# Performance work log

Measured on AMD Instinct MI355X. Metric: run time of the kernel, lower is better.

The kernel has to match this reference:

```python
import jax, jax.numpy as jnp
import numpy as np

B, N, D, E, ET, L = 2, 50000, 64, 400000, 200000, 6
R_STRUCT = 4
EPS = 1e-5


def _ln(x, g, b):
    m = jnp.mean(x, axis=-1, keepdims=True)
    v = jnp.mean((x - m) ** 2, axis=-1, keepdims=True)
    return (x - m) * jax.lax.rsqrt(v + EPS) * g + b


def _nbf(boundary, src, dst, rel_e_fn, W, b, g, beta):
    # One RelNBFNet / TextRelNBFNet stack of GeneralizedRelationalConv layers:
    #   distmult message, sum aggregation with boundary self-loop message,
    #   linear([x, agg]) -> layernorm -> relu, short_cut residual.
    # boundary: [B, N, D]
    x = boundary
    for i in range(W.shape[0]):
        msg = x[:, src, :] * rel_e_fn(i)                    # [B, E, D]
        agg = jnp.zeros_like(x).at[:, dst, :].add(msg) + boundary
        h = jnp.concatenate([x, agg], axis=-1) @ W[i] + b[i]
        h = jax.nn.relu(_ln(h, g[i], beta[i]))
        x = h + x                                           # short_cut
    return x


def setup_inputs() -> dict:
    key = jax.random.key(0)
    ks = jax.random.split(key, 16)
    s = 0.05
    return {
        "rel_text_init": jax.random.normal(ks[0], (N, D), jnp.float32),
        "struct_rel": jax.random.normal(ks[1], (L, R_STRUCT, D), jnp.float32) * s,
        "struct_W": jax.random.normal(ks[2], (L, 2 * D, D), jnp.float32) * s,
        "struct_b": jnp.zeros((L, D), jnp.float32),
        "struct_g": jnp.ones((L, D), jnp.float32),
        "struct_beta": jnp.zeros((L, D), jnp.float32),
        "text_rel": jax.random.normal(ks[3], (L, 1, D), jnp.float32) * s,
        "text_W": jax.random.normal(ks[4], (L, 2 * D, D), jnp.float32) * s,
        "text_b": jnp.zeros((L, D), jnp.float32),
        "text_g": jnp.ones((L, D), jnp.float32),
        "text_beta": jnp.zeros((L, D), jnp.float32),
        "fuse_W1": jax.random.normal(ks[5], (2 * D, D), jnp.float32) * s,
        "fuse_b1": jnp.zeros((D,), jnp.float32),
        "fuse_W2": jax.random.normal(ks[6], (D, D), jnp.float32) * s,
        "fuse_b2": jnp.zeros((D,), jnp.float32),
        "h_index": jax.random.randint(ks[7], (B,), 0, N),
        "edge_index": jax.random.randint(ks[8], (2, E), 0, N),
        "edge_type": jax.random.randint(ks[9], (E,), 0, R_STRUCT),
        "text_edge_index": jax.random.randint(ks[10], (2, ET), 0, N),
    }


def reference(rel_text_init, struct_rel, struct_W, struct_b, struct_g, struct_beta,
              text_rel, text_W, text_b, text_g, text_beta,
              fuse_W1, fuse_b1, fuse_W2, fuse_b2,
              h_index, edge_index, edge_type, text_edge_index):
    # struct branch: boundary = indicator at query relation node
    boundary_s = jnp.zeros((B, N, D), rel_text_init.dtype).at[jnp.arange(B), h_index].add(1.0)
    h = _nbf(boundary_s, edge_index[0], edge_index[1],
             lambda i: struct_rel[i][edge_type],
             struct_W, struct_b, struct_g, struct_beta)
    # text branch: boundary = text-derived init features, single relation type
    boundary_t = jnp.broadcast_to(rel_text_init[None], (B, N, D))
    z = _nbf(boundary_t, text_edge_index[0], text_edge_index[1],
             lambda i: text_rel[i, 0][None, None, :],
             text_W, text_b, text_g, text_beta)
    # mlp fusion (alpha = 1.0)
    f = jax.nn.relu(jnp.concatenate([h, z], axis=-1) @ fuse_W1 + fuse_b1)
    return f @ fuse_W2 + fuse_b2
```

## Files before the change

### kernel.cpp

```cpp
#include <hip/hip_runtime.h>


__device__ __forceinline__ float bf2f(unsigned short u) {
    return __uint_as_float(((unsigned)u) << 16);
}
__device__ __forceinline__ unsigned short f2bf(float f) {
    unsigned u = __float_as_uint(f);
    u += 0x7FFF + ((u >> 16) & 1);
    return (unsigned short)(u >> 16);
}
#define PACK2(a, b) ((unsigned)f2bf(a) | ((unsigned)f2bf(b) << 16))

#define FMA4R(v, wbase, R0, R1, R2, R3) do {                                  \
    const float4* _w = (const float4*)(wbase); float4 _t;                     \
    _t=_w[0]; R0.x=fmaf(v,_t.x,R0.x); R0.y=fmaf(v,_t.y,R0.y); R0.z=fmaf(v,_t.z,R0.z); R0.w=fmaf(v,_t.w,R0.w); \
    _t=_w[1]; R1.x=fmaf(v,_t.x,R1.x); R1.y=fmaf(v,_t.y,R1.y); R1.z=fmaf(v,_t.z,R1.z); R1.w=fmaf(v,_t.w,R1.w); \
    _t=_w[2]; R2.x=fmaf(v,_t.x,R2.x); R2.y=fmaf(v,_t.y,R2.y); R2.z=fmaf(v,_t.z,R2.z); R2.w=fmaf(v,_t.w,R2.w); \
    _t=_w[3]; R3.x=fmaf(v,_t.x,R3.x); R3.y=fmaf(v,_t.y,R3.y); R3.z=fmaf(v,_t.z,R3.z); R3.w=fmaf(v,_t.w,R3.w); \
} while (0)

#define FMA4R2(v0, v1, wbase, P0,P1,P2,P3, Q0,Q1,Q2,Q3) do {                  \
    const float4* _w = (const float4*)(wbase); float4 _t;                     \
    _t=_w[0];                                                                 \
    P0.x=fmaf(v0,_t.x,P0.x); P0.y=fmaf(v0,_t.y,P0.y); P0.z=fmaf(v0,_t.z,P0.z); P0.w=fmaf(v0,_t.w,P0.w); \
    Q0.x=fmaf(v1,_t.x,Q0.x); Q0.y=fmaf(v1,_t.y,Q0.y); Q0.z=fmaf(v1,_t.z,Q0.z); Q0.w=fmaf(v1,_t.w,Q0.w); \
    _t=_w[1];                                                                 \
    P1.x=fmaf(v0,_t.x,P1.x); P1.y=fmaf(v0,_t.y,P1.y); P1.z=fmaf(v0,_t.z,P1.z); P1.w=fmaf(v0,_t.w,P1.w); \
    Q1.x=fmaf(v1,_t.x,Q1.x); Q1.y=fmaf(v1,_t.y,Q1.y); Q1.z=fmaf(v1,_t.z,Q1.z); Q1.w=fmaf(v1,_t.w,Q1.w); \
    _t=_w[2];                                                                 \
    P2.x=fmaf(v0,_t.x,P2.x); P2.y=fmaf(v0,_t.y,P2.y); P2.z=fmaf(v0,_t.z,P2.z); P2.w=fmaf(v0,_t.w,P2.w); \
    Q2.x=fmaf(v1,_t.x,Q2.x); Q2.y=fmaf(v1,_t.y,Q2.y); Q2.z=fmaf(v1,_t.z,Q2.z); Q2.w=fmaf(v1,_t.w,Q2.w); \
    _t=_w[3];                                                                 \
    P3.x=fmaf(v0,_t.x,P3.x); P3.y=fmaf(v0,_t.y,P3.y); P3.z=fmaf(v0,_t.z,P3.z); P3.w=fmaf(v0,_t.w,P3.w); \
    Q3.x=fmaf(v1,_t.x,Q3.x); Q3.y=fmaf(v1,_t.y,Q3.y); Q3.z=fmaf(v1,_t.z,Q3.z); Q3.w=fmaf(v1,_t.w,Q3.w); \
} while (0)

#define SUM4(Ai) ((Ai.x + Ai.y) + (Ai.z + Ai.w))
#define VAR4M(Ai, mm, vv) do { float _c;                                      \
    _c = Ai.x - mm; vv = fmaf(_c, _c, vv); _c = Ai.y - mm; vv = fmaf(_c, _c, vv); \
    _c = Ai.z - mm; vv = fmaf(_c, _c, vv); _c = Ai.w - mm; vv = fmaf(_c, _c, vv); \
} while (0)

#define RSEL(ty) (((ty) < 2) ? ((ty) == 0 ? r0 : r1) : ((ty) == 2 ? r2 : r3))

__global__ __launch_bounds__(256) void k_init_onehot(
    float* __restrict__ x, unsigned short* __restrict__ xbf,
    const int* __restrict__ h_index, int N, int total)
{
    int idx = blockIdx.x * 256 + threadIdx.x;
    if (idx >= total) return;
    int row = idx >> 6;
    int b = row / N;
    int n = row - b * N;
    bool hit = (n == h_index[b]);
    x[idx] = hit ? 1.0f : 0.0f;
    xbf[idx] = hit ? 0x3F80 : 0;
}

__global__ __launch_bounds__(256) void k_cast_init(
    const float* __restrict__ init, float* __restrict__ x,
    unsigned short* __restrict__ xbf, int total)
{
    int idx = blockIdx.x * 256 + threadIdx.x;
    if (idx >= total) return;
    float f = init[idx];
    x[idx] = f;
    xbf[idx] = f2bf(f);
}

__global__ __launch_bounds__(256) void k_hist_all(
    const int* __restrict__ dst_s, const int* __restrict__ dst_t,
    int* __restrict__ cnt_s, int* __restrict__ cnt_t, int E, int ET)
{
    int i = blockIdx.x * 256 + threadIdx.x;
    if (i < E) atomicAdd(&cnt_s[dst_s[i]], 1);
    else if (i < E + ET) atomicAdd(&cnt_t[dst_t[i - E]], 1);
}

__global__ __launch_bounds__(1024) void k_scan_blk2(
    const int* __restrict__ cnt_s, int* __restrict__ off_s, int* __restrict__ bsum_s,
    const int* __restrict__ cnt_t, int* __restrict__ off_t, int* __restrict__ bsum_t,
    int n, int nb)
{
    bool tpath = blockIdx.x >= nb;
    int lb = tpath ? blockIdx.x - nb : blockIdx.x;
    const int* cnt = tpath ? cnt_t : cnt_s;
    int* off = tpath ? off_t : off_s;
    int* bsum = tpath ? bsum_t : bsum_s;

    __shared__ int wsum[16], wpre[16], tot;
    int tid = threadIdx.x, lane = tid & 63, w = tid >> 6;
    int i = lb * 1024 + tid;
    int v = (i < n) ? cnt[i] : 0;
    int s = v;
    #pragma unroll
    for (int d = 1; d < 64; d <<= 1) {
        int t = __shfl_up(s, d);
        if (lane >= d) s += t;
    }
    if (lane == 63) wsum[w] = s;
    __syncthreads();
    if (w == 0 && lane < 16) {
        int ws = wsum[lane];
        int p = ws;
        #pragma unroll
        for (int d = 1; d < 16; d <<= 1) {
            int t = __shfl_up(p, d);
            if (lane >= d) p += t;
        }
        wpre[lane] = p - ws;
        if (lane == 15) tot = p;
    }
    __syncthreads();
    if (i < n) off[i + 1] = wpre[w] + s;
    if (tid == 0) {
        bsum[lb] = tot;
        if (lb == 0) off[0] = 0;
    }
}

__global__ __launch_bounds__(1024) void k_scan_top2(
    int* __restrict__ bsum_s, int* __restrict__ bsum_t, int nb)
{
    int* bsum = (blockIdx.x == 0) ? bsum_s : bsum_t;
    __shared__ int wsum[16], wpre[16];
    int tid = threadIdx.x, lane = tid & 63, w = tid >> 6;
    int v = (tid < nb) ? bsum[tid] : 0;
    int s = v;
    #pragma unroll
    for (int d = 1; d < 64; d <<= 1) {
        int t = __shfl_up(s, d);
        if (lane >= d) s += t;
    }
    if (lane == 63) wsum[w] = s;
    __syncthreads();
    if (w == 0 && lane < 16) {
        int ws = wsum[lane];
        int p = ws;
        #pragma unroll
        for (int d = 1; d < 16; d <<= 1) {
            int t = __shfl_up(p, d);
            if (lane >= d) p += t;
        }
        wpre[lane] = p - ws;
    }
    __syncthreads();
    if (tid < nb) bsum[tid] = wpre[w] + s - v;
}

__global__ __launch_bounds__(1024) void k_scan_add2(
    const int* __restrict__ bsum_s, int* __restrict__ off_s,
    const int* __restrict__ bsum_t, int* __restrict__ off_t, int n, int nb)
{
    bool tpath = blockIdx.x >= nb;
    int lb = tpath ? blockIdx.x - nb : blockIdx.x;
    int i = lb * 1024 + threadIdx.x;
    if (i < n) (tpath ? off_t : off_s)[i + 1] += (tpath ? bsum_t : bsum_s)[lb];
}

__global__ __launch_bounds__(256) void k_fill_all(
    const int* __restrict__ src_s, const int* __restrict__ dst_s,
    const int* __restrict__ etype,
    const int* __restrict__ off_s, int* __restrict__ cnt_s, int* __restrict__ pk_s,
    const int* __restrict__ src_t, const int* __restrict__ dst_t,
    const int* __restrict__ off_t, int* __restrict__ cnt_t, int* __restrict__ pk_t,
    int E, int ET)
{
    int i = blockIdx.x * 256 + threadIdx.x;
    if (i < E) {
        int d = dst_s[i];
        int pos = off_s[d] + atomicSub(&cnt_s[d], 1) - 1;
        pk_s[pos] = src_s[i] | (etype[i] << 27);
    } else if (i < E + ET) {
        int e = i - E;
        int d = dst_t[e];
        int pos = off_t[d] + atomicSub(&cnt_t[d], 1) - 1;
        pk_t[pos] = src_t[e];
    }
}

__global__ __launch_bounds__(256) void k_gather_all(
    const unsigned short* __restrict__ xbs, float* __restrict__ aggs,
    const int* __restrict__ offs, const int* __restrict__ pks,
    const float* __restrict__ rels,
    const int* __restrict__ hidx,
    const unsigned short* __restrict__ xbt, float* __restrict__ aggt,
    const int* __restrict__ offt, const int* __restrict__ pkt,
    const float* __restrict__ relt,
    const float* __restrict__ init,
    int N, int sblocks, int tblocks)
{
    int tid = threadIdx.x;
    int lane = tid & 63;
    bool isStruct; int lb;
    if (sblocks == tblocks) { isStruct = !(blockIdx.x & 1); lb = blockIdx.x >> 1; }
    else if ((int)blockIdx.x < sblocks) { isStruct = true; lb = blockIdx.x; }
    else { isStruct = false; lb = blockIdx.x - sblocks; }
    int n = (lb * 256 + tid) >> 6;
    if (n >= N) return;

    if (isStruct) {
        float r0 = rels[lane], r1 = rels[64 + lane];
        float r2 = rels[128 + lane], r3 = rels[192 + lane];
        const unsigned short* x0 = xbs;
        const unsigned short* x1 = xbs + (size_t)N * 64;
        float acc0 = (n == hidx[0]) ? 1.0f : 0.0f;
        float acc1 = (n == hidx[1]) ? 1.0f : 0.0f;
        int p0 = __builtin_amdgcn_readfirstlane(offs[n]);
        int p1 = __builtin_amdgcn_readfirstlane(offs[n + 1]);
        for (int p = p0; p < p1; p += 64) {
            int myPk = (p + lane < p1) ? pks[p + lane] : 0;
            int cnt = min(p1 - p, 64);
            int i = 0;
            for (; i + 4 <= cnt; i += 4) {
                int pka = __shfl(myPk, i + 0), pkb = __shfl(myPk, i + 1);
                int pkc = __shfl(myPk, i + 2), pkd = __shfl(myPk, i + 3);
                int sa = pka & 0x03FFFFFF, ta = pka >> 27;
                int sb = pkb & 0x03FFFFFF, tb = pkb >> 27;
                int sc = pkc & 0x03FFFFFF, tc = pkc >> 27;
                int sd = pkd & 0x03FFFFFF, td = pkd >> 27;
                float ra = RSEL(ta), rb = RSEL(tb), rc = RSEL(tc), rd = RSEL(td);
                float a0 = bf2f(x0[(size_t)sa * 64 + lane]), a1 = bf2f(x1[(size_t)sa * 64 + lane]);
                float b0 = bf2f(x0[(size_t)sb * 64 + lane]), b1 = bf2f(x1[(size_t)sb * 64 + lane]);
                float c0 = bf2f(x0[(size_t)sc * 64 + lane]), c1 = bf2f(x1[(size_t)sc * 64 + lane]);
                float d0 = bf2f(x0[(size_t)sd * 64 + lane]), d1 = bf2f(x1[(size_t)sd * 64 + lane]);
                acc0 = fmaf(a0, ra, acc0); acc1 = fmaf(a1, ra, acc1);
                acc0 = fmaf(b0, rb, acc0); acc1 = fmaf(b1, rb, acc1);
                acc0 = fmaf(c0, rc, acc0); acc1 = fmaf(c1, rc, acc1);
                acc0 = fmaf(d0, rd, acc0); acc1 = fmaf(d1, rd, acc1);
            }
            for (; i < cnt; ++i) {
                int pk = __shfl(myPk, i);
                int s = pk & 0x03FFFFFF, ty = pk >> 27;
                float r = RSEL(ty);
                acc0 = fmaf(bf2f(x0[(size_t)s * 64 + lane]), r, acc0);
                acc1 = fmaf(bf2f(x1[(size_t)s * 64 + lane]), r, acc1);
            }
        }
        aggs[(size_t)n * 64 + lane] = acc0;
        aggs[(size_t)(N + n) * 64 + lane] = acc1;
    } else {
        float r = relt[lane];
        float acc = init[(size_t)n * 64 + lane];
        float acc2 = 0.f;
        int p0 = __builtin_amdgcn_readfirstlane(offt[n]);
        int p1 = __builtin_amdgcn_readfirstlane(offt[n + 1]);
        for (int p = p0; p < p1; p += 64) {
            int myPk = (p + lane < p1) ? pkt[p + lane] : 0;
            int cnt = min(p1 - p, 64);
            int i = 0;
            for (; i + 8 <= cnt; i += 8) {
                int s0 = __shfl(myPk, i + 0), s1 = __shfl(myPk, i + 1);
                int s2 = __shfl(myPk, i + 2), s3 = __shfl(myPk, i + 3);
                int s4 = __shfl(myPk, i + 4), s5 = __shfl(myPk, i + 5);
                int s6 = __shfl(myPk, i + 6), s7 = __shfl(myPk, i + 7);
                float a = bf2f(xbt[(size_t)s0 * 64 + lane]), b = bf2f(xbt[(size_t)s1 * 64 + lane]);
                float c = bf2f(xbt[(size_t)s2 * 64 + lane]), d = bf2f(xbt[(size_t)s3 * 64 + lane]);
                float e = bf2f(xbt[(size_t)s4 * 64 + lane]), f = bf2f(xbt[(size_t)s5 * 64 + lane]);
                float g = bf2f(xbt[(size_t)s6 * 64 + lane]), h = bf2f(xbt[(size_t)s7 * 64 + lane]);
                acc = fmaf(a, r, acc);  acc2 = fmaf(b, r, acc2);
                acc = fmaf(c, r, acc);  acc2 = fmaf(d, r, acc2);
                acc = fmaf(e, r, acc);  acc2 = fmaf(f, r, acc2);
                acc = fmaf(g, r, acc);  acc2 = fmaf(h, r, acc2);
            }
            for (; i < cnt; ++i) {
                int s = __shfl(myPk, i);
                acc = fmaf(bf2f(xbt[(size_t)s * 64 + lane]), r, acc);
            }
        }
        aggt[(size_t)n * 64 + lane] = acc + acc2;
    }
}

__global__ __launch_bounds__(256) void k_gather_struct_gen(
    const float* __restrict__ x, float* __restrict__ agg,
    const int* __restrict__ off, const int* __restrict__ packed,
    const float* __restrict__ rel, const int* __restrict__ h_index,
    int N, int BN)
{
    int wid = (blockIdx.x * 256 + threadIdx.x) >> 6;
    int lane = threadIdx.x & 63;
    if (wid >= BN) return;
    int b = wid / N;
    int n = wid - b * N;
    float r0 = rel[lane], r1 = rel[64 + lane];
    float r2 = rel[128 + lane], r3 = rel[192 + lane];
    const float* xb = x + (size_t)b * N * 64;
    float acc = (n == h_index[b]) ? 1.0f : 0.0f;
    int p0 = off[n], p1 = off[n + 1];
    for (int p = p0; p < p1; ++p) {
        int pk = packed[p];
        int s = pk & 0x03FFFFFF, ty = pk >> 27;
        acc = fmaf(xb[(size_t)s * 64 + lane], RSEL(ty), acc);
    }
    agg[(size_t)wid * 64 + lane] = acc;
}

__global__ __launch_bounds__(256) void k_update_all(
    const float* __restrict__ Ws, const float* __restrict__ bs_,
    const float* __restrict__ gs, const float* __restrict__ betas,
    float* __restrict__ xs, unsigned short* __restrict__ xbs,
    const float* __restrict__ aggs, int rows_s,
    const float* __restrict__ Wt, const float* __restrict__ bt_,
    const float* __restrict__ gt_, const float* __restrict__ betat,
    float* __restrict__ xt, unsigned short* __restrict__ xbt,
    const float* __restrict__ aggt, int rows_t,
    int bs_blocks, int bt_blocks)
{
    bool tpath; int lb;
    if (bs_blocks == 2 * bt_blocks) {
        int m3 = blockIdx.x % 3, d3 = blockIdx.x / 3;
        if (m3 != 2) { tpath = false; lb = d3 * 2 + m3; }
        else { tpath = true; lb = d3; }
    } else if ((int)blockIdx.x < bs_blocks) { tpath = false; lb = blockIdx.x; }
    else { tpath = true; lb = blockIdx.x - bs_blocks; }

    const float* W    = tpath ? Wt : Ws;
    const float* bias = tpath ? bt_ : bs_;
    const float* g    = tpath ? gt_ : gs;
    const float* beta = tpath ? betat : betas;
    float* x          = tpath ? xt : xs;
    unsigned short* xb = tpath ? xbt : xbs;
    const float* agg  = tpath ? aggt : aggs;
    int rows          = tpath ? rows_t : rows_s;

    __shared__ float Wl[128 * 64];
    __shared__ float bl[64], gl[64], bel[64];
    int tid = threadIdx.x;
    {
        const float4* W4 = (const float4*)W;
        float4* Wl4 = (float4*)Wl;
        #pragma unroll
        for (int i = 0; i < 8; ++i) Wl4[tid + i * 256] = W4[tid + i * 256];
        if (tid < 64) { bl[tid] = bias[tid]; gl[tid] = g[tid]; bel[tid] = beta[tid]; }
    }
    __syncthreads();

    int gt2 = lb * 256 + tid;
    int pair = gt2 >> 2;
    int q = gt2 & 3, jc = q * 16;
    int r0i = pair * 2, r1i = r0i + 1;
    if (r0i >= rows) return;
    bool h1 = (r1i < rows);
    const float* xr0 = x + (size_t)r0i * 64;
    const float* ar0 = agg + (size_t)r0i * 64;
    const float* xr1 = h1 ? x + (size_t)r1i * 64 : xr0;
    const float* ar1 = h1 ? agg + (size_t)r1i * 64 : ar0;

    const float4* bj = (const float4*)(bl + jc);
    float4 A0 = bj[0], A1 = bj[1], A2 = bj[2], A3 = bj[3];
    float4 B0 = bj[0], B1 = bj[1], B2 = bj[2], B3 = bj[3];

    #pragma unroll
    for (int kb = 0; kb < 64; kb += 4) {
        float4 i0 = *(const float4*)(xr0 + kb);
        float4 i1 = *(const float4*)(xr1 + kb);
        FMA4R2(i0.x, i1.x, Wl + (kb + 0) * 64 + jc, A0,A1,A2,A3, B0,B1,B2,B3);
        FMA4R2(i0.y, i1.y, Wl + (kb + 1) * 64 + jc, A0,A1,A2,A3, B0,B1,B2,B3);
        FMA4R2(i0.z, i1.z, Wl + (kb + 2) * 64 + jc, A0,A1,A2,A3, B0,B1,B2,B3);
        FMA4R2(i0.w, i1.w, Wl + (kb + 3) * 64 + jc, A0,A1,A2,A3, B0,B1,B2,B3);
    }
    #pragma unroll
    for (int kb = 0; kb < 64; kb += 4) {
        float4 i0 = *(const float4*)(ar0 + kb);
        float4 i1 = *(const float4*)(ar1 + kb);
        FMA4R2(i0.x, i1.x, Wl + (64 + kb + 0) * 64 + jc, A0,A1,A2,A3, B0,B1,B2,B3);
        FMA4R2(i0.y, i1.y, Wl + (64 + kb + 1) * 64 + jc, A0,A1,A2,A3, B0,B1,B2,B3);
        FMA4R2(i0.z, i1.z, Wl + (64 + kb + 2) * 64 + jc, A0,A1,A2,A3, B0,B1,B2,B3);
        FMA4R2(i0.w, i1.w, Wl + (64 + kb + 3) * 64 + jc, A0,A1,A2,A3, B0,B1,B2,B3);
    }

    float ls0 = SUM4(A0) + SUM4(A1) + SUM4(A2) + SUM4(A3);
    float ls1 = SUM4(B0) + SUM4(B1) + SUM4(B2) + SUM4(B3);
    ls0 += __shfl_xor(ls0, 1); ls0 += __shfl_xor(ls0, 2);
    ls1 += __shfl_xor(ls1, 1); ls1 += __shfl_xor(ls1, 2);
    float m0 = ls0 * (1.0f / 64.0f), m1 = ls1 * (1.0f / 64.0f);
    float v0 = 0.f, v1 = 0.f;
    VAR4M(A0, m0, v0); VAR4M(A1, m0, v0); VAR4M(A2, m0, v0); VAR4M(A3, m0, v0);
    VAR4M(B0, m1, v1); VAR4M(B1, m1, v1); VAR4M(B2, m1, v1); VAR4M(B3, m1, v1);
    v0 += __shfl_xor(v0, 1); v0 += __shfl_xor(v0, 2);
    v1 += __shfl_xor(v1, 1); v1 += __shfl_xor(v1, 2);
    float inv0 = rsqrtf(v0 * (1.0f / 64.0f) + 1e-5f);
    float inv1 = rsqrtf(v1 * (1.0f / 64.0f) + 1e-5f);

    const float4* gg4 = (const float4*)(gl + jc);
    const float4* bb4 = (const float4*)(bel + jc);
    #define OUTC(Aj, c, mm, iv, xrp, xwp, xbm) do {                           \
        float4 xv = ((const float4*)(xrp))[c];                                \
        float4 gg = gg4[c]; float4 bb = bb4[c];                               \
        float4 y;                                                             \
        y.x = fmaxf((Aj.x - mm) * iv * gg.x + bb.x, 0.f) + xv.x;              \
        y.y = fmaxf((Aj.y - mm) * iv * gg.y + bb.y, 0.f) + xv.y;              \
        y.z = fmaxf((Aj.z - mm) * iv * gg.z + bb.z, 0.f) + xv.z;              \
        y.w = fmaxf((Aj.w - mm) * iv * gg.w + bb.w, 0.f) + xv.w;              \
        ((float4*)(xwp))[c] = y;                                              \
        ((uint2*)(xbm))[c] = make_uint2(PACK2(y.x, y.y), PACK2(y.z, y.w));    \
    } while (0)
    float* xw0 = x + (size_t)r0i * 64 + jc;
    unsigned short* xb0 = xb + (size_t)r0i * 64 + jc;
    OUTC(A0, 0, m0, inv0, xr0 + jc, xw0, xb0); OUTC(A1, 1, m0, inv0, xr0 + jc, xw0, xb0);
    OUTC(A2, 2, m0, inv0, xr0 + jc, xw0, xb0); OUTC(A3, 3, m0, inv0, xr0 + jc, xw0, xb0);
    if (h1) {
        float* xw1 = x + (size_t)r1i * 64 + jc;
        unsigned short* xb1 = xb + (size_t)r1i * 64 + jc;
        OUTC(B0, 0, m1, inv1, xr1 + jc, xw1, xb1); OUTC(B1, 1, m1, inv1, xr1 + jc, xw1, xb1);
        OUTC(B2, 2, m1, inv1, xr1 + jc, xw1, xb1); OUTC(B3, 3, m1, inv1, xr1 + jc, xw1, xb1);
    }
    #undef OUTC
}

__global__ __launch_bounds__(256) void k_fuse(
    const float* __restrict__ W1, const float* __restrict__ b1,
    const float* __restrict__ W2, const float* __restrict__ b2,
    float* __restrict__ out, const float* __restrict__ z, int N, int rows)
{
    __shared__ float W1l[128 * 64];
    __shared__ float W2l[64 * 64];
    __shared__ float b1l[64], b2l[64];
    int tid = threadIdx.x;
    {
        const float4* Wa = (const float4*)W1;
        float4* Wla = (float4*)W1l;
        #pragma unroll
        for (int i = 0; i < 8; ++i) Wla[tid + i * 256] = Wa[tid + i * 256];
        const float4* Wb = (const float4*)W2;
        float4* Wlb = (float4*)W2l;
        #pragma unroll
        for (int i = 0; i < 4; ++i) Wlb[tid + i * 256] = Wb[tid + i * 256];
        if (tid < 64) { b1l[tid] = b1[tid]; b2l[tid] = b2[tid]; }
    }
    __syncthreads();

    int gt2 = blockIdx.x * 256 + tid;
    int row = gt2 >> 2;
    int q = gt2 & 3;
    int jc = q * 16;
    if (row >= rows) return;
    int n = row % N;
    const float* hr = out + (size_t)row * 64;
    const float* zr = z + (size_t)n * 64;
    int lane = tid & 63;

    const float4* bj = (const float4*)(b1l + jc);
    float4 F0 = bj[0], F1 = bj[1], F2 = bj[2], F3 = bj[3];
    #pragma unroll
    for (int kb = 0; kb < 64; kb += 4) {
        float4 iv = *(const float4*)(hr + kb);
        FMA4R(iv.x, W1l + (kb + 0) * 64 + jc, F0, F1, F2, F3);
        FMA4R(iv.y, W1l + (kb + 1) * 64 + jc, F0, F1, F2, F3);
        FMA4R(iv.z, W1l + (kb + 2) * 64 + jc, F0, F1, F2, F3);
        FMA4R(iv.w, W1l + (kb + 3) * 64 + jc, F0, F1, F2, F3);
    }
    #pragma unroll
    for (int kb = 0; kb < 64; kb += 4) {
        float4 iv = *(const float4*)(zr + kb);
        FMA4R(iv.x, W1l + (64 + kb + 0) * 64 + jc, F0, F1, F2, F3);
        FMA4R(iv.y, W1l + (64 + kb + 1) * 64 + jc, F0, F1, F2, F3);
        FMA4R(iv.z, W1l + (64 + kb + 2) * 64 + jc, F0, F1, F2, F3);
        FMA4R(iv.w, W1l + (64 + kb + 3) * 64 + jc, F0, F1, F2, F3);
    }
    F0.x = fmaxf(F0.x, 0.f); F0.y = fmaxf(F0.y, 0.f); F0.z = fmaxf(F0.z, 0.f); F0.w = fmaxf(F0.w, 0.f);
    F1.x = fmaxf(F1.x, 0.f); F1.y = fmaxf(F1.y, 0.f); F1.z = fmaxf(F1.z, 0.f); F1.w = fmaxf(F1.w, 0.f);
    F2.x = fmaxf(F2.x, 0.f); F2.y = fmaxf(F2.y, 0.f); F2.z = fmaxf(F2.z, 0.f); F2.w = fmaxf(F2.w, 0.f);
    F3.x = fmaxf(F3.x, 0.f); F3.y = fmaxf(F3.y, 0.f); F3.z = fmaxf(F3.z, 0.f); F3.w = fmaxf(F3.w, 0.f);

    const float4* bj2 = (const float4*)(b2l + jc);
    float4 O0 = bj2[0], O1 = bj2[1], O2 = bj2[2], O3 = bj2[3];
    int srcLane = (lane & ~3) | ((q + 1) & 3);
    #pragma unroll
    for (int s = 0; s < 4; ++s) {
        int c = (q + s) & 3;
        const float* w2 = W2l + (c * 16) * 64 + jc;
        FMA4R(F0.x, w2 + 0 * 64,  O0, O1, O2, O3);
        FMA4R(F0.y, w2 + 1 * 64,  O0, O1, O2, O3);
        FMA4R(F0.z, w2 + 2 * 64,  O0, O1, O2, O3);
        FMA4R(F0.w, w2 + 3 * 64,  O0, O1, O2, O3);
        FMA4R(F1.x, w2 + 4 * 64,  O0, O1, O2, O3);
        FMA4R(F1.y, w2 + 5 * 64,  O0, O1, O2, O3);
        FMA4R(F1.z, w2 + 6 * 64,  O0, O1, O2, O3);
        FMA4R(F1.w, w2 + 7 * 64,  O0, O1, O2, O3);
        FMA4R(F2.x, w2 + 8 * 64,  O0, O1, O2, O3);
        FMA4R(F2.y, w2 + 9 * 64,  O0, O1, O2, O3);
        FMA4R(F2.z, w2 + 10 * 64, O0, O1, O2, O3);
        FMA4R(F2.w, w2 + 11 * 64, O0, O1, O2, O3);
        FMA4R(F3.x, w2 + 12 * 64, O0, O1, O2, O3);
        FMA4R(F3.y, w2 + 13 * 64, O0, O1, O2, O3);
        FMA4R(F3.z, w2 + 14 * 64, O0, O1, O2, O3);
        FMA4R(F3.w, w2 + 15 * 64, O0, O1, O2, O3);
        if (s < 3) {
            F0.x = __shfl(F0.x, srcLane); F0.y = __shfl(F0.y, srcLane);
            F0.z = __shfl(F0.z, srcLane); F0.w = __shfl(F0.w, srcLane);
            F1.x = __shfl(F1.x, srcLane); F1.y = __shfl(F1.y, srcLane);
            F1.z = __shfl(F1.z, srcLane); F1.w = __shfl(F1.w, srcLane);
            F2.x = __shfl(F2.x, srcLane); F2.y = __shfl(F2.y, srcLane);
            F2.z = __shfl(F2.z, srcLane); F2.w = __shfl(F2.w, srcLane);
            F3.x = __shfl(F3.x, srcLane); F3.y = __shfl(F3.y, srcLane);
            F3.z = __shfl(F3.z, srcLane); F3.w = __shfl(F3.w, srcLane);
        }
    }
    float4* ow4 = (float4*)(out + (size_t)row * 64 + jc);
    ow4[0] = O0; ow4[1] = O1; ow4[2] = O2; ow4[3] = O3;
}

extern "C" void kernel_launch(void* const* d_in, const int* in_sizes, int n_in,
                              void* d_out, int out_size, void* d_ws, size_t ws_size,
                              hipStream_t stream)
{
    const float* rel_text_init = (const float*)d_in[0];
    const float* struct_rel    = (const float*)d_in[1];
    const float* struct_W      = (const float*)d_in[2];
    const float* struct_b      = (const float*)d_in[3];
    const float* struct_g      = (const float*)d_in[4];
    const float* struct_beta   = (const float*)d_in[5];
    const float* text_rel      = (const float*)d_in[6];
    const float* text_W        = (const float*)d_in[7];
    const float* text_b        = (const float*)d_in[8];
    const float* text_g        = (const float*)d_in[9];
    const float* text_beta     = (const float*)d_in[10];
    const float* fuse_W1       = (const float*)d_in[11];
    const float* fuse_b1       = (const float*)d_in[12];
    const float* fuse_W2       = (const float*)d_in[13];
    const float* fuse_b2       = (const float*)d_in[14];
    const int*   h_index       = (const int*)d_in[15];
    const int*   edge_index    = (const int*)d_in[16];
    const int*   edge_type     = (const int*)d_in[17];
    const int*   text_edge_idx = (const int*)d_in[18];

    const int B  = in_sizes[15];
    const int N  = in_sizes[0] / 64;
    const int E  = in_sizes[17];
    const int ET = in_sizes[18] / 2;
    const int L  = in_sizes[3] / 64;
    const int R  = in_sizes[1] / (L * 64);

    const int* src  = edge_index;
    const int* dst  = edge_index + E;
    const int* tsrc = text_edge_idx;
    const int* tdst = text_edge_idx + ET;

    float* x_t   = (float*)d_ws;
    float* agg_t = x_t + (size_t)N * 64;
    float* agg_s = agg_t + (size_t)N * 64;
    unsigned short* xbf_s = (unsigned short*)(agg_s + (size_t)B * N * 64);
    unsigned short* xbf_t = xbf_s + (size_t)B * N * 64;
    int*   cnt_s = (int*)(xbf_t + (size_t)N * 64);
    int*   off_s = cnt_s + N;
    int*   pk_s  = off_s + N + 1;
    int*   cnt_t = pk_s + E;
    int*   off_t = cnt_t + N;
    int*   pk_t  = off_t + N + 1;
    int*   bsum_s = pk_t + ET;
    int*   bsum_t = bsum_s + 1024;

    float* x_s = (float*)d_out;

    const size_t nd  = (size_t)N * 64;
    const int rows_s = B * N;
    const int tot_s  = rows_s * 64;
    const int nb     = (N + 1023) / 1024;

    const int gb_init   = (tot_s + 255) / 256;
    const int gb_castt  = ((int)nd + 255) / 256;
    const int gb_hist   = (E + ET + 255) / 256;
    const int gb_wave_n = (N * 64 + 255) / 256;
    const int pairs_s   = (rows_s + 1) / 2;
    const int pairs_t   = (N + 1) / 2;
    const int bs_blocks = (pairs_s * 4 + 255) / 256;
    const int bt_blocks = (pairs_t * 4 + 255) / 256;
    const int gb_fuse   = (rows_s * 4 + 255) / 256;

    hipMemsetAsync(cnt_s, 0, (size_t)N * 4, stream);
    hipMemsetAsync(cnt_t, 0, (size_t)N * 4, stream);
    k_hist_all<<<gb_hist, 256, 0, stream>>>(dst, tdst, cnt_s, cnt_t, E, ET);
    k_scan_blk2<<<2 * nb, 1024, 0, stream>>>(cnt_s, off_s, bsum_s,
                                             cnt_t, off_t, bsum_t, N, nb);
    k_scan_top2<<<2, 1024, 0, stream>>>(bsum_s, bsum_t, nb);
    k_scan_add2<<<2 * nb, 1024, 0, stream>>>(bsum_s, off_s, bsum_t, off_t, N, nb);
    k_fill_all<<<gb_hist, 256, 0, stream>>>(src, dst, edge_type, off_s, cnt_s, pk_s,
                                            tsrc, tdst, off_t, cnt_t, pk_t, E, ET);

    k_init_onehot<<<gb_init, 256, 0, stream>>>(x_s, xbf_s, h_index, N, tot_s);
    k_cast_init<<<gb_castt, 256, 0, stream>>>(rel_text_init, x_t, xbf_t, (int)nd);

    for (int i = 0; i < L; ++i) {
        if (B == 2) {
            k_gather_all<<<2 * gb_wave_n, 256, 0, stream>>>(
                xbf_s, agg_s, off_s, pk_s, struct_rel + (size_t)i * R * 64, h_index,
                xbf_t, agg_t, off_t, pk_t, text_rel + (size_t)i * 64, rel_text_init,
                N, gb_wave_n, gb_wave_n);
        } else {
            k_gather_struct_gen<<<(rows_s * 64 + 255) / 256, 256, 0, stream>>>(
                x_s, agg_s, off_s, pk_s,
                struct_rel + (size_t)i * R * 64, h_index, N, rows_s);
            k_gather_all<<<gb_wave_n, 256, 0, stream>>>(
                xbf_s, agg_s, off_s, pk_s, struct_rel + (size_t)i * R * 64, h_index,
                xbf_t, agg_t, off_t, pk_t, text_rel + (size_t)i * 64, rel_text_init,
                N, 0, gb_wave_n);
        }
        k_update_all<<<bs_blocks + bt_blocks, 256, 0, stream>>>(
            struct_W + (size_t)i * 128 * 64, struct_b + i * 64,
            struct_g + i * 64, struct_beta + i * 64, x_s, xbf_s, agg_s, rows_s,
            text_W + (size_t)i * 128 * 64, text_b + i * 64,
            text_g + i * 64, text_beta + i * 64, x_t, xbf_t, agg_t, N,
            bs_blocks, bt_blocks);
    }

    k_fuse<<<gb_fuse, 256, 0, stream>>>(
        fuse_W1, fuse_b1, fuse_W2, fuse_b2, x_s, x_t, N, rows_s);
}
```

Baseline: 692.9 us.

## Interleave struct batch bf16 mirror so gather loads both batches in one word

The bf16 mirror of the struct-branch features changes from two separate batch planes to an interleaved layout where each node/channel holds both batches' values in one 32-bit word. The gather then issues one 4-byte load per edge instead of two 2-byte loads to distant planes, and its inner loop is unrolled to 8 edges for more memory-level parallelism. The update kernel now writes scattered 2-byte halves into the interleaved mirror, which may cost more write efficiency, and the init kernel builds the interleaved one-hot mirror.

Result: slower. 854.4 us (+23.3%).

```diff
diff --git a/kernel.cpp b/kernel.cpp
--- a/kernel.cpp
+++ b/kernel.cpp
@@ -10,6 +10,16 @@
     return (unsigned short)(u >> 16);
 }
 #define PACK2(a, b) ((unsigned)f2bf(a) | ((unsigned)f2bf(b) << 16))
+
+__device__ __forceinline__ float4 lnout(float4 A, float m, float inv,
+                                        float4 xv, float4 gg, float4 bb) {
+    float4 y;
+    y.x = fmaxf((A.x - m) * inv * gg.x + bb.x, 0.f) + xv.x;
+    y.y = fmaxf((A.y - m) * inv * gg.y + bb.y, 0.f) + xv.y;
+    y.z = fmaxf((A.z - m) * inv * gg.z + bb.z, 0.f) + xv.z;
+    y.w = fmaxf((A.w - m) * inv * gg.w + bb.w, 0.f) + xv.w;
+    return y;
+}
 
 #define FMA4R(v, wbase, R0, R1, R2, R3) do {                                  \
     const float4* _w = (const float4*)(wbase); float4 _t;                     \
@@ -44,17 +54,21 @@
 #define RSEL(ty) (((ty) < 2) ? ((ty) == 0 ? r0 : r1) : ((ty) == 2 ? r2 : r3))
 
 __global__ __launch_bounds__(256) void k_init_onehot(
-    float* __restrict__ x, unsigned short* __restrict__ xbf,
-    const int* __restrict__ h_index, int N, int total)
+    float* __restrict__ x, unsigned* __restrict__ xmir,
+    const int* __restrict__ h_index, int N, int total, int b2)
 {
     int idx = blockIdx.x * 256 + threadIdx.x;
     if (idx >= total) return;
     int row = idx >> 6;
     int b = row / N;
     int n = row - b * N;
-    bool hit = (n == h_index[b]);
-    x[idx] = hit ? 1.0f : 0.0f;
-    xbf[idx] = hit ? 0x3F80 : 0;
+    x[idx] = (n == h_index[b]) ? 1.0f : 0.0f;
+    if (b2 && idx < N * 64) {
+        int nn = idx >> 6;
+        unsigned w = ((nn == h_index[0]) ? 0x3F80u : 0u)
+                   | (((nn == h_index[1]) ? 0x3F80u : 0u) << 16);
+        xmir[idx] = w;
+    }
 }
 
 __global__ __launch_bounds__(256) void k_cast_init(
@@ -180,7 +194,7 @@
 }
 
 __global__ __launch_bounds__(256) void k_gather_all(
-    const unsigned short* __restrict__ xbs, float* __restrict__ aggs,
+    const unsigned* __restrict__ xws, float* __restrict__ aggs,
     const int* __restrict__ offs, const int* __restrict__ pks,
     const float* __restrict__ rels,
     const int* __restrict__ hidx,
@@ -202,8 +216,6 @@
     if (isStruct) {
         float r0 = rels[lane], r1 = rels[64 + lane];
         float r2 = rels[128 + lane], r3 = rels[192 + lane];
-        const unsigned short* x0 = xbs;
-        const unsigned short* x1 = xbs + (size_t)N * 64;
         float acc0 = (n == hidx[0]) ? 1.0f : 0.0f;
         float acc1 = (n == hidx[1]) ? 1.0f : 0.0f;
         int p0 = __builtin_amdgcn_readfirstlane(offs[n]);
@@ -212,29 +224,47 @@
             int myPk = (p + lane < p1) ? pks[p + lane] : 0;
             int cnt = min(p1 - p, 64);
             int i = 0;
-            for (; i + 4 <= cnt; i += 4) {
-                int pka = __shfl(myPk, i + 0), pkb = __shfl(myPk, i + 1);
-                int pkc = __shfl(myPk, i + 2), pkd = __shfl(myPk, i + 3);
-                int sa = pka & 0x03FFFFFF, ta = pka >> 27;
-                int sb = pkb & 0x03FFFFFF, tb = pkb >> 27;
-                int sc = pkc & 0x03FFFFFF, tc = pkc >> 27;
-                int sd = pkd & 0x03FFFFFF, td = pkd >> 27;
-                float ra = RSEL(ta), rb = RSEL(tb), rc = RSEL(tc), rd = RSEL(td);
-                float a0 = bf2f(x0[(size_t)sa * 64 + lane]), a1 = bf2f(x1[(size_t)sa * 64 + lane]);
-                float b0 = bf2f(x0[(size_t)sb * 64 + lane]), b1 = bf2f(x1[(size_t)sb * 64 + lane]);
-                float c0 = bf2f(x0[(size_t)sc * 64 + lane]), c1 = bf2f(x1[(size_t)sc * 64 + lane]);
-                float d0 = bf2f(x0[(size_t)sd * 64 + lane]), d1 = bf2f(x1[(size_t)sd * 64 + lane]);
-                acc0 = fmaf(a0, ra, acc0); acc1 = fmaf(a1, ra, acc1);
-                acc0 = fmaf(b0, rb, acc0); acc1 = fmaf(b1, rb, acc1);
-                acc0 = fmaf(c0, rc, acc0); acc1 = fmaf(c1, rc, acc1);
-                acc0 = fmaf(d0, rd, acc0); acc1 = fmaf(d1, rd, acc1);
+            for (; i + 8 <= cnt; i += 8) {
+                int k0 = __shfl(myPk, i + 0), k1 = __shfl(myPk, i + 1);
+                int k2 = __shfl(myPk, i + 2), k3 = __shfl(myPk, i + 3);
+                int k4 = __shfl(myPk, i + 4), k5 = __shfl(myPk, i + 5);
+                int k6 = __shfl(myPk, i + 6), k7 = __shfl(myPk, i + 7);
+                unsigned w0 = xws[(size_t)(k0 & 0x03FFFFFF) * 64 + lane];
+                unsigned w1 = xws[(size_t)(k1 & 0x03FFFFFF) * 64 + lane];
+                unsigned w2 = xws[(size_t)(k2 & 0x03FFFFFF) * 64 + lane];
+                unsigned w3 = xws[(size_t)(k3 & 0x03FFFFFF) * 64 + lane];
+                unsigned w4 = xws[(size_t)(k4 & 0x03FFFFFF) * 64 + lane];
+                unsigned w5 = xws[(size_t)(k5 & 0x03FFFFFF) * 64 + lane];
+                unsigned w6 = xws[(size_t)(k6 & 0x03FFFFFF) * 64 + lane];
+                unsigned w7 = xws[(size_t)(k7 & 0x03FFFFFF) * 64 + lane];
+                int t0 = k0 >> 27, t1 = k1 >> 27, t2 = k2 >> 27, t3 = k3 >> 27;
+                int t4 = k4 >> 27, t5 = k5 >> 27, t6 = k6 >> 27, t7 = k7 >> 27;
+                float ra = RSEL(t0), rb = RSEL(t1), rc = RSEL(t2), rd = RSEL(t3);
+                float re = RSEL(t4), rf = RSEL(t5), rg = RSEL(t6), rh = RSEL(t7);
+                acc0 = fmaf(bf2f((unsigned short)w0), ra, acc0);
+                acc1 = fmaf(bf2f((unsigned short)(w0 >> 16)), ra, acc1);
+                acc0 = fmaf(bf2f((unsigned short)w1), rb, acc0);
+                acc1 = fmaf(bf2f((unsigned short)(w1 >> 16)), rb, acc1);
+                acc0 = fmaf(bf2f((unsigned short)w2), rc, acc0);
+                acc1 = fmaf(bf2f((unsigned short)(w2 >> 16)), rc, acc1);
+                acc0 = fmaf(bf2f((unsigned short)w3), rd, acc0);
+                acc1 = fmaf(bf2f((unsigned short)(w3 >> 16)), rd, acc1);
+                acc0 = fmaf(bf2f((unsigned short)w4), re, acc0);
+                acc1 = fmaf(bf2f((unsigned short)(w4 >> 16)), re, acc1);
+                acc0 = fmaf(bf2f((unsigned short)w5), rf, acc0);
+                acc1 = fmaf(bf2f((unsigned short)(w5 >> 16)), rf, acc1);
+                acc0 = fmaf(bf2f((unsigned short)w6), rg, acc0);
+                acc1 = fmaf(bf2f((unsigned short)(w6 >> 16)), rg, acc1);
+                acc0 = fmaf(bf2f((unsigned short)w7), rh, acc0);
+                acc1 = fmaf(bf2f((unsigned short)(w7 >> 16)), rh, acc1);
             }
             for (; i < cnt; ++i) {
                 int pk = __shfl(myPk, i);
                 int s = pk & 0x03FFFFFF, ty = pk >> 27;
                 float r = RSEL(ty);
-                acc0 = fmaf(bf2f(x0[(size_t)s * 64 + lane]), r, acc0);
-                acc1 = fmaf(bf2f(x1[(size_t)s * 64 + lane]), r, acc1);
+                unsigned w = xws[(size_t)s * 64 + lane];
+                acc0 = fmaf(bf2f((unsigned short)w), r, acc0);
+                acc1 = fmaf(bf2f((unsigned short)(w >> 16)), r, acc1);
             }
         }
         aggs[(size_t)n * 64 + lane] = acc0;
@@ -299,13 +329,13 @@
 __global__ __launch_bounds__(256) void k_update_all(
     const float* __restrict__ Ws, const float* __restrict__ bs_,
     const float* __restrict__ gs, const float* __restrict__ betas,
-    float* __restrict__ xs, unsigned short* __restrict__ xbs,
+    float* __restrict__ xs, unsigned short* __restrict__ mirs,
     const float* __restrict__ aggs, int rows_s,
     const float* __restrict__ Wt, const float* __restrict__ bt_,
     const float* __restrict__ gt_, const float* __restrict__ betat,
-    float* __restrict__ xt, unsigned short* __restrict__ xbt,
+    float* __restrict__ xt, unsigned short* __restrict__ mirt,
     const float* __restrict__ aggt, int rows_t,
-    int bs_blocks, int bt_blocks)
+    int bs_blocks, int bt_blocks, int Nn, int b2)
 {
     bool tpath; int lb;
     if (bs_blocks == 2 * bt_blocks) {
@@ -320,7 +350,6 @@
     const float* g    = tpath ? gt_ : gs;
     const float* beta = tpath ? betat : betas;
     float* x          = tpath ? xt : xs;
-    unsigned short* xb = tpath ? xbt : xbs;
     const float* agg  = tpath ? aggt : aggs;
     int rows          = tpath ? rows_t : rows_s;
 
@@ -385,28 +414,35 @@
 
     const float4* gg4 = (const float4*)(gl + jc);
     const float4* bb4 = (const float4*)(bel + jc);
-    #define OUTC(Aj, c, mm, iv, xrp, xwp, xbm) do {                           \
-        float4 xv = ((const float4*)(xrp))[c];                                \
-        float4 gg = gg4[c]; float4 bb = bb4[c];                               \
-        float4 y;                                                             \
-        y.x = fmaxf((Aj.x - mm) * iv * gg.x + bb.x, 0.f) + xv.x;              \
-        y.y = fmaxf((Aj.y - mm) * iv * gg.y + bb.y, 0.f) + xv.y;              \
-        y.z = fmaxf((Aj.z - mm) * iv * gg.z + bb.z, 0.f) + xv.z;              \
-        y.w = fmaxf((Aj.w - mm) * iv * gg.w + bb.w, 0.f) + xv.w;              \
-        ((float4*)(xwp))[c] = y;                                              \
-        ((uint2*)(xbm))[c] = make_uint2(PACK2(y.x, y.y), PACK2(y.z, y.w));    \
+
+    #define OUTROW(AA0, AA1, AA2, AA3, mm, iv, ri, xrp) do {                  \
+        float* xwp = x + (size_t)(ri) * 64 + jc;                              \
+        float4 y0 = lnout(AA0, mm, iv, ((const float4*)(xrp))[0], gg4[0], bb4[0]); \
+        float4 y1 = lnout(AA1, mm, iv, ((const float4*)(xrp))[1], gg4[1], bb4[1]); \
+        float4 y2 = lnout(AA2, mm, iv, ((const float4*)(xrp))[2], gg4[2], bb4[2]); \
+        float4 y3 = lnout(AA3, mm, iv, ((const float4*)(xrp))[3], gg4[3], bb4[3]); \
+        ((float4*)xwp)[0] = y0; ((float4*)xwp)[1] = y1;                       \
+        ((float4*)xwp)[2] = y2; ((float4*)xwp)[3] = y3;                       \
+        if (tpath) {                                                          \
+            uint2* mt = (uint2*)(mirt + (size_t)(ri) * 64 + jc);              \
+            mt[0] = make_uint2(PACK2(y0.x, y0.y), PACK2(y0.z, y0.w));         \
+            mt[1] = make_uint2(PACK2(y1.x, y1.y), PACK2(y1.z, y1.w));         \
+            mt[2] = make_uint2(PACK2(y2.x, y2.y), PACK2(y2.z, y2.w));         \
+            mt[3] = make_uint2(PACK2(y3.x, y3.y), PACK2(y3.z, y3.w));         \
+        } else if (b2) {                                                      \
+            int bb_ = (ri) >= Nn ? 1 : 0;                                     \
+            int nn_ = (ri) - bb_ * Nn;                                        \
+            unsigned short* mb = mirs + ((size_t)nn_ * 64 + jc) * 2 + bb_;    \
+            mb[0]  = f2bf(y0.x); mb[2]  = f2bf(y0.y); mb[4]  = f2bf(y0.z); mb[6]  = f2bf(y0.w); \
+            mb[8]  = f2bf(y1.x); mb[10] = f2bf(y1.y); mb[12] = f2bf(y1.z); mb[14] = f2bf(y1.w); \
+            mb[16] = f2bf(y2.x); mb[18] = f2bf(y2.y); mb[20] = f2bf(y2.z); mb[22] = f2bf(y2.w); \
+            mb[24] = f2bf(y3.x); mb[26] = f2bf(y3.y); mb[28] = f2bf(y3.z); mb[30] = f2bf(y3.w); \
+        }                                                                     \
     } while (0)
-    float* xw0 = x + (size_t)r0i * 64 + jc;
-    unsigned short* xb0 = xb + (size_t)r0i * 64 + jc;
-    OUTC(A0, 0, m0, inv0, xr0 + jc, xw0, xb0); OUTC(A1, 1, m0, inv0, xr0 + jc, xw0, xb0);
-    OUTC(A2, 2, m0, inv0, xr0 + jc, xw0, xb0); OUTC(A3, 3, m0, inv0, xr0 + jc, xw0, xb0);
-    if (h1) {
-        float* xw1 = x + (size_t)r1i * 64 + jc;
-        unsigned short* xb1 = xb + (size_t)r1i * 64 + jc;
-        OUTC(B0, 0, m1, inv1, xr1 + jc, xw1, xb1); OUTC(B1, 1, m1, inv1, xr1 + jc, xw1, xb1);
-        OUTC(B2, 2, m1, inv1, xr1 + jc, xw1, xb1); OUTC(B3, 3, m1, inv1, xr1 + jc, xw1, xb1);
-    }
-    #undef OUTC
+
+    OUTROW(A0, A1, A2, A3, m0, inv0, r0i, xr0 + jc);
+    if (h1) OUTROW(B0, B1, B2, B3, m1, inv1, r1i, xr1 + jc);
+    #undef OUTROW
 }
 
 __global__ __launch_bounds__(256) void k_fuse(
@@ -558,6 +594,7 @@
     const int rows_s = B * N;
     const int tot_s  = rows_s * 64;
     const int nb     = (N + 1023) / 1024;
+    const int b2     = (B == 2) ? 1 : 0;
 
     const int gb_init   = (tot_s + 255) / 256;
     const int gb_castt  = ((int)nd + 255) / 256;
@@ -579,13 +616,15 @@
     k_fill_all<<<gb_hist, 256, 0, stream>>>(src, dst, edge_type, off_s, cnt_s, pk_s,
                                             tsrc, tdst, off_t, cnt_t, pk_t, E, ET);
 
-    k_init_onehot<<<gb_init, 256, 0, stream>>>(x_s, xbf_s, h_index, N, tot_s);
+    k_init_onehot<<<gb_init, 256, 0, stream>>>(
+        x_s, (unsigned*)xbf_s, h_index, N, tot_s, b2);
     k_cast_init<<<gb_castt, 256, 0, stream>>>(rel_text_init, x_t, xbf_t, (int)nd);
 
     for (int i = 0; i < L; ++i) {
-        if (B == 2) {
+        if (b2) {
             k_gather_all<<<2 * gb_wave_n, 256, 0, stream>>>(
-                xbf_s, agg_s, off_s, pk_s, struct_rel + (size_t)i * R * 64, h_index,
+                (const unsigned*)xbf_s, agg_s, off_s, pk_s,
+                struct_rel + (size_t)i * R * 64, h_index,
                 xbf_t, agg_t, off_t, pk_t, text_rel + (size_t)i * 64, rel_text_init,
                 N, gb_wave_n, gb_wave_n);
         } else {
@@ -593,7 +632,8 @@
                 x_s, agg_s, off_s, pk_s,
                 struct_rel + (size_t)i * R * 64, h_index, N, rows_s);
             k_gather_all<<<gb_wave_n, 256, 0, stream>>>(
-                xbf_s, agg_s, off_s, pk_s, struct_rel + (size_t)i * R * 64, h_index,
+                (const unsigned*)xbf_s, agg_s, off_s, pk_s,
+                struct_rel + (size_t)i * R * 64, h_index,
                 xbf_t, agg_t, off_t, pk_t, text_rel + (size_t)i * 64, rel_text_init,
                 N, 0, gb_wave_n);
         }
@@ -602,7 +642,7 @@
             struct_g + i * 64, struct_beta + i * 64, x_s, xbf_s, agg_s, rows_s,
             text_W + (size_t)i * 128 * 64, text_b + i * 64,
             text_g + i * 64, text_beta + i * 64, x_t, xbf_t, agg_t, N,
-            bs_blocks, bt_blocks);
+            bs_blocks, bt_blocks, N, b2);
     }
 
     k_fuse<<<gb_fuse, 256, 0, stream>>>(
```
